# Performance work log

Measured on AMD Instinct MI355X. Metric: run time of the kernel, lower is better.

## Reference

```python
import jax, jax.numpy as jnp
import numpy as np
from jax import lax

ROI_H = 8        # _ROI_HEIGHT
MAX_BOX = 32     # generator.MAX_BOX
MAX_LEN = 64     # static cap on pooled width/height (replaces dynamic max_width)
SCALE = 8.0      # feature_map_scale
IOU_THR = 0.5    # tf.image.non_max_suppression default
SCORE_THR = 0.3
B, H, W, C = 4, 64, 64, 128


def _reconstruct_boxes(b, scale):
    # b: [B,H,W,4] per-pixel (l,t,r,b) offsets -> absolute (x1,y1,x2,y2) * scale
    Hd, Wd = b.shape[1], b.shape[2]
    xx = jnp.arange(Wd, dtype=b.dtype)[None, None, :]
    yy = jnp.arange(Hd, dtype=b.dtype)[None, :, None]
    left = xx - b[..., 0]
    top = yy - b[..., 1]
    right = xx + b[..., 2]
    bottom = yy + b[..., 3]
    return scale * jnp.stack([left, top, right, bottom], axis=-1)


def _nms_single(bbs, ss):
    # greedy NMS, bbs: [N,4] (x1,y1,x2,y2), ss: [N]; returns [MAX_BOX,4]
    x1, y1, x2, y2 = bbs[:, 0], bbs[:, 1], bbs[:, 2], bbs[:, 3]
    areas = (x2 - x1) * (y2 - y1)

    def body(i, state):
        valid, sel = state
        m = jnp.where(valid, ss, -jnp.inf)
        j = jnp.argmax(m)
        ok = m[j] > -jnp.inf
        sel = sel.at[i].set(jnp.where(ok, j.astype(jnp.int32), -1))
        bj = bbs[j]
        iw = jnp.maximum(jnp.minimum(x2, bj[2]) - jnp.maximum(x1, bj[0]), 0.0)
        ih = jnp.maximum(jnp.minimum(y2, bj[3]) - jnp.maximum(y1, bj[1]), 0.0)
        inter = iw * ih
        iou = inter / (areas + areas[j] - inter + 1e-9)
        valid = valid & (iou <= IOU_THR)   # selected box self-suppresses (iou=1)
        return valid, sel

    N = bbs.shape[0]
    valid0 = jnp.ones((N,), dtype=bool)
    sel0 = jnp.full((MAX_BOX,), -1, dtype=jnp.int32)
    _, sel = lax.fori_loop(0, MAX_BOX, body, (valid0, sel0))
    ok = sel >= 0
    idx = jnp.maximum(sel, 0)
    sb = bbs[idx]
    sc = ss[idx]
    keep = ok & (sc >= SCORE_THR)
    return jnp.where(keep[:, None], sb, jnp.zeros_like(sb))


def _bilinear(img, x, y):
    # img [H,W,C], x [Wp], y [Hp] -> [Hp,Wp,C]; matches TF clip-then-weight behavior
    Hh, Ww = img.shape[0], img.shape[1]
    x0f = jnp.floor(x)
    y0f = jnp.floor(y)
    x0 = jnp.clip(x0f.astype(jnp.int32), 0, Ww - 1)
    x1 = jnp.clip(x0f.astype(jnp.int32) + 1, 0, Ww - 1)
    y0 = jnp.clip(y0f.astype(jnp.int32), 0, Hh - 1)
    y1 = jnp.clip(y0f.astype(jnp.int32) + 1, 0, Hh - 1)
    Ia = img[y0[:, None], x0[None, :]]
    Ib = img[y0[:, None], x1[None, :]]
    Ic = img[y1[:, None], x0[None, :]]
    Id = img[y1[:, None], x1[None, :]]
    x0v, x1v = x0.astype(img.dtype), x1.astype(img.dtype)
    y0v, y1v = y0.astype(img.dtype), y1.astype(img.dtype)
    wa = (x1v - x)[None, :] * (y1v - y)[:, None]
    wb = (x1v - x)[None, :] * (y - y0v)[:, None]
    wc = (x - x0v)[None, :] * (y1v - y)[:, None]
    wd = (x - x0v)[None, :] * (y - y0v)[:, None]
    return (Ia * wa[..., None] + Ib * wb[..., None]
            + Ic * wc[..., None] + Id * wd[..., None])


def _pool_one(img, box, horizontal):
    # img [H,W,C], box [4] in feature-map coords
    w = box[2] - box[0]
    h = box[3] - box[1]
    is_dir = (w >= h) if horizontal else (w < h)
    bz = jnp.where(is_dir, box, jnp.zeros_like(box))
    w = bz[2] - bz[0]
    h = bz[3] - bz[1]
    non_zero = (w >= 0.1) | (h >= 0.1)
    bw = jnp.where(w <= 0.0, 1e-4, w)
    bh = jnp.where(h <= 0.0, 1e-4, h)
    ratio = jnp.where(non_zero, (bw / bh) if horizontal else (bh / bw), 0.0)
    n = jnp.minimum(jnp.ceil(ratio * ROI_H), float(MAX_LEN)).astype(jnp.int32)
    length_f = jnp.maximum(n.astype(img.dtype), 2.0)  # guard div-by-zero for masked boxes
    fmask = non_zero.astype(img.dtype)
    if horizontal:
        map_w = bw / (length_f - 1.0)
        map_h = bh / (ROI_H - 1.0)
        xx = jnp.arange(MAX_LEN, dtype=img.dtype) * map_w + bz[0]
        yy = jnp.arange(ROI_H, dtype=img.dtype) * map_h + bz[1]
        pooled = _bilinear(img, xx, yy)                     # [ROI_H, MAX_LEN, C]
        colmask = (jnp.arange(MAX_LEN) < n).astype(img.dtype) * fmask
        pooled = pooled * colmask[None, :, None]
    else:
        map_w = bw / (ROI_H - 1.0)
        map_h = bh / (length_f - 1.0)
        xx = jnp.arange(ROI_H, dtype=img.dtype) * map_w + bz[0]
        yy = jnp.arange(MAX_LEN, dtype=img.dtype) * map_h + bz[1]
        pooled = _bilinear(img, xx, yy)                     # [MAX_LEN, ROI_H, C]
        rowmask = (jnp.arange(MAX_LEN) < n).astype(img.dtype) * fmask
        pooled = pooled * rowmask[:, None, None]
    return pooled, n


def _roi_pool(fmap, boxes, horizontal):
    # fmap [B,H,W,C], boxes [B,M,4] -> ([B,M,...], [B,M])
    per_img = lambda img, bxs: jax.vmap(lambda b: _pool_one(img, b, horizontal))(bxs)
    return jax.vmap(per_img)(fmap, boxes)


def setup_inputs() -> dict:
    key = jax.random.key(0)
    k1, k2 = jax.random.split(key)
    fmap = jax.random.normal(k1, (B, H, W, C), dtype=jnp.float32)
    # channel 0 -> score logit, channels 1:5 -> positive l/t/r/b offsets in fmap px
    bbox_output = jax.random.uniform(k2, (B, H, W, 5), dtype=jnp.float32) * 3.0
    return {"fmap": fmap, "bbox_output": bbox_output}


def reference(fmap, bbox_output):
    scores = jax.nn.sigmoid(bbox_output[..., 0])                  # [B,H,W]
    boxes = _reconstruct_boxes(bbox_output[..., 1:5], SCALE)      # [B,H,W,4]
    Bn = scores.shape[0]
    bbs = boxes.reshape(Bn, -1, 4)
    ss = scores.reshape(Bn, -1)
    nms_boxes = jax.vmap(_nms_single)(bbs, ss)                    # [B,MAX_BOX,4]
    fb = nms_boxes / SCALE                                        # back to fmap coords
    h_roi, widths = _roi_pool(fmap, fb, True)    # [B,M,8,MAX_LEN,C], [B,M]
    v_roi, heights = _roi_pool(fmap, fb, False)  # [B,M,MAX_LEN,8,C], [B,M]
    return nms_boxes, h_roi, widths, v_roi, heights
```

## Files before the change

### kernel.cpp

```cpp
#include <hip/hip_runtime.h>
#include <hip/hip_bf16.h>
#include <math.h>

#pragma clang fp contract(off)

#define NPIX 4096
#define MAXB 32
#define NB   4
#define ROI_N 8388608
#define OTOT (ROI_N / 8)

__global__ __launch_bounds__(256) void nms_kernel(const float* __restrict__ bbox,
                                                  float* __restrict__ out_nms,
                                                  float* __restrict__ params,
                                                  float* __restrict__ out_w,
                                                  float* __restrict__ out_hh)
{
    const int b = blockIdx.x;
    const int t = threadIdx.x;

    __shared__ float s_box[NPIX][4];
    __shared__ float s_sel[MAXB][4];
    __shared__ float s_red[2][4][2];

    float rs[16], rx1[16], ry1[16], rx2[16], ry2[16], rar[16];

    const float* src = bbox + (size_t)b * NPIX * 5;

    #pragma unroll
    for (int i = 0; i < 16; ++i) {
        int p = i * 256 + t;
        int y = p >> 6, x = p & 63;
        float c0 = src[p * 5 + 0];
        float c1 = src[p * 5 + 1];
        float c2 = src[p * 5 + 2];
        float c3 = src[p * 5 + 3];
        float c4 = src[p * 5 + 4];
        float sc = 1.0f / (1.0f + expf(-c0));
        float x1 = 8.0f * ((float)x - c1);
        float y1 = 8.0f * ((float)y - c2);
        float x2 = 8.0f * ((float)x + c3);
        float y2 = 8.0f * ((float)y + c4);
        rs[i] = sc;
        rx1[i] = x1; ry1[i] = y1; rx2[i] = x2; ry2[i] = y2;
        rar[i] = (x2 - x1) * (y2 - y1);
        s_box[p][0] = x1; s_box[p][1] = y1; s_box[p][2] = x2; s_box[p][3] = y2;
    }
    __syncthreads();

    unsigned valid = 0xFFFFu;
    float wx1 = -1e30f, wy1 = -1e30f, wx2 = -1e30f, wy2 = -1e30f, warea = 0.f;

    for (int it = 0; it < MAXB; ++it) {
        float best = -INFINITY;
        int   bidx = 0x7FFFFFFF;
        #pragma unroll
        for (int i = 0; i < 16; ++i) {
            float iw = fmaxf(fminf(rx2[i], wx2) - fmaxf(rx1[i], wx1), 0.f);
            float ih = fmaxf(fminf(ry2[i], wy2) - fmaxf(ry1[i], wy1), 0.f);
            float inter = iw * ih;
            float iou = __fdiv_rn(inter, rar[i] + warea - inter + 1e-9f);
            valid &= ~(((iou > 0.5f) ? 1u : 0u) << i);
            float vv = ((valid >> i) & 1u) ? rs[i] : -INFINITY;
            bool take = vv > best;
            bidx = take ? (i * 256 + t) : bidx;
            best = take ? vv : best;
        }
        #pragma unroll
        for (int off = 32; off; off >>= 1) {
            float ov = __shfl_xor(best, off);
            int   oi = __shfl_xor(bidx, off);
            bool take = (ov > best) || (ov == best && oi < bidx);
            best = take ? ov : best;
            bidx = take ? oi : bidx;
        }
        int buf = it & 1;
        if ((t & 63) == 0) {
            s_red[buf][t >> 6][0] = best;
            s_red[buf][t >> 6][1] = __int_as_float(bidx);
        }
        __syncthreads();
        best = s_red[buf][0][0]; bidx = __float_as_int(s_red[buf][0][1]);
        #pragma unroll
        for (int wv = 1; wv < 4; ++wv) {
            float ov = s_red[buf][wv][0];
            int   oi = __float_as_int(s_red[buf][wv][1]);
            bool take = (ov > best) || (ov == best && oi < bidx);
            best = take ? ov : best;
            bidx = take ? oi : bidx;
        }

        int jj = min(bidx, NPIX - 1);
        wx1 = s_box[jj][0]; wy1 = s_box[jj][1];
        wx2 = s_box[jj][2]; wy2 = s_box[jj][3];
        warea = (wx2 - wx1) * (wy2 - wy1);

        if (t == 0) {
            bool keep = (best >= 0.3f);
            float o0 = keep ? wx1 : 0.f, o1 = keep ? wy1 : 0.f;
            float o2 = keep ? wx2 : 0.f, o3 = keep ? wy2 : 0.f;
            float* o = out_nms + ((size_t)b * MAXB + it) * 4;
            o[0] = o0; o[1] = o1; o[2] = o2; o[3] = o3;
            s_sel[it][0] = o0; s_sel[it][1] = o1;
            s_sel[it][2] = o2; s_sel[it][3] = o3;
        }
    }
    __syncthreads();

    if (t < 64) {
        int dir = t >> 5, bx = t & 31;
        float x1 = s_sel[bx][0] * 0.125f, y1 = s_sel[bx][1] * 0.125f;
        float x2 = s_sel[bx][2] * 0.125f, y2 = s_sel[bx][3] * 0.125f;
        float w = x2 - x1, h = y2 - y1;
        bool is_dir = (dir == 0) ? (w >= h) : (w < h);
        if (!is_dir) { x1 = 0.f; y1 = 0.f; x2 = 0.f; y2 = 0.f; }
        w = x2 - x1; h = y2 - y1;
        bool  non_zero = (w >= 0.1f) || (h >= 0.1f);
        float bw = (w <= 0.f) ? 1e-4f : w;
        float bh = (h <= 0.f) ? 1e-4f : h;
        float ratio = non_zero ? ((dir == 0) ? __fdiv_rn(bw, bh) : __fdiv_rn(bh, bw)) : 0.f;
        int   n = (int)fminf(ceilf(ratio * 8.0f), 64.0f);
        float length_f = fmaxf((float)n, 2.0f);
        float fmask = non_zero ? 1.f : 0.f;
        float map_w, map_h;
        if (dir == 0) { map_w = __fdiv_rn(bw, length_f - 1.0f); map_h = __fdiv_rn(bh, 7.0f); }
        else          { map_w = __fdiv_rn(bw, 7.0f);            map_h = __fdiv_rn(bh, length_f - 1.0f); }
        int gtb = b * MAXB + bx;
        float* P = params + ((size_t)dir * 128 + gtb) * 8;
        P[0] = x1; P[1] = y1; P[2] = map_w; P[3] = map_h;
        P[4] = (float)n; P[5] = fmask; P[6] = 0.f; P[7] = 0.f;
        ((dir == 0) ? out_w : out_hh)[gtb] = (float)n;
    }
}

__global__ __launch_bounds__(256) void roi_kernel(const float* __restrict__ fmap,
                                                  const float* __restrict__ params,
                                                  float* __restrict__ out_h,
                                                  float* __restrict__ out_v)
{
    int idx = blockIdx.x * 256 + threadIdx.x;
    int dir = (idx >= OTOT) ? 1 : 0;
    int e   = idx - dir * OTOT;
    int tb  = e >> 13;
    int within = e & 8191;
    int pos = within >> 4;
    int ch8 = within & 15;

    const float4* P4 = (const float4*)(params + ((size_t)dir * 128 + tb) * 8);
    float4 p0 = P4[0];
    float4 p1 = P4[1];
    float bz0x = p0.x, bz0y = p0.y, map_w = p0.z, map_h = p0.w;
    int   n     = (int)p1.x;
    float fmask = p1.y;

    int rr, cc; float mask;
    if (dir == 0) { rr = pos >> 6; cc = pos & 63; mask = (cc < n) ? fmask : 0.f; }
    else          { rr = pos >> 3; cc = pos & 7;  mask = (rr < n) ? fmask : 0.f; }

    int el = (tb << 16) | (pos << 7) | (ch8 << 3);
    float* outp = ((dir == 0) ? out_h : out_v) + el;

    if (mask == 0.f) {
        float4 z = make_float4(0.f, 0.f, 0.f, 0.f);
        *(float4*)outp = z;
        *(float4*)(outp + 4) = z;
        return;
    }

    float x = __fadd_rn(__fmul_rn((float)cc, map_w), bz0x);
    float y = __fadd_rn(__fmul_rn((float)rr, map_h), bz0y);

    float x0f = floorf(x), y0f = floorf(y);
    int ix0 = min(max((int)x0f,     0), 63);
    int ix1 = min(max((int)x0f + 1, 0), 63);
    int iy0 = min(max((int)y0f,     0), 63);
    int iy1 = min(max((int)y0f + 1, 0), 63);

    const float* img = fmap + ((size_t)(tb >> 5)) * (64 * 64 * 128) + (ch8 << 3);
    const float* pa = img + (iy0 * 64 + ix0) * 128;
    const float* pb = img + (iy0 * 64 + ix1) * 128;
    const float* pc = img + (iy1 * 64 + ix0) * 128;
    const float* pd = img + (iy1 * 64 + ix1) * 128;
    float4 Ia0 = *(const float4*)pa,       Ia1 = *(const float4*)(pa + 4);
    float4 Ib0 = *(const float4*)pb,       Ib1 = *(const float4*)(pb + 4);
    float4 Ic0 = *(const float4*)pc,       Ic1 = *(const float4*)(pc + 4);
    float4 Id0 = *(const float4*)pd,       Id1 = *(const float4*)(pd + 4);

    float x0v = (float)ix0, x1v = (float)ix1;
    float y0v = (float)iy0, y1v = (float)iy1;
    float wa = (x1v - x) * (y1v - y);
    float wb = (x1v - x) * (y - y0v);
    float wc = (x - x0v) * (y1v - y);
    float wd = (x - x0v) * (y - y0v);

    float4 o0, o1;
    o0.x = (Ia0.x * wa + Ib0.x * wb + Ic0.x * wc + Id0.x * wd) * mask;
    o0.y = (Ia0.y * wa + Ib0.y * wb + Ic0.y * wc + Id0.y * wd) * mask;
    o0.z = (Ia0.z * wa + Ib0.z * wb + Ic0.z * wc + Id0.z * wd) * mask;
    o0.w = (Ia0.w * wa + Ib0.w * wb + Ic0.w * wc + Id0.w * wd) * mask;
    o1.x = (Ia1.x * wa + Ib1.x * wb + Ic1.x * wc + Id1.x * wd) * mask;
    o1.y = (Ia1.y * wa + Ib1.y * wb + Ic1.y * wc + Id1.y * wd) * mask;
    o1.z = (Ia1.z * wa + Ib1.z * wb + Ic1.z * wc + Id1.z * wd) * mask;
    o1.w = (Ia1.w * wa + Ib1.w * wb + Ic1.w * wc + Id1.w * wd) * mask;
    *(float4*)outp = o0;
    *(float4*)(outp + 4) = o1;
}

extern "C" void kernel_launch(void* const* d_in, const int* in_sizes, int n_in,
                              void* d_out, int out_size, void* d_ws, size_t ws_size,
                              hipStream_t stream) {
    const float* fmap = (const float*)d_in[0];
    const float* bbox = (const float*)d_in[1];
    float* out = (float*)d_out;

    float* out_nms = out;
    float* out_h   = out + 512;
    float* out_w   = out_h + ROI_N;
    float* out_v   = out_w + 128;
    float* out_hh  = out_v + ROI_N;

    float* params = (float*)d_ws;

    nms_kernel<<<NB, 256, 0, stream>>>(bbox, out_nms, params, out_w, out_hh);
    roi_kernel<<<(2 * OTOT) / 256, 256, 0, stream>>>(fmap, params, out_h, out_v);
}
```

Baseline: 139.6 us.

## Use lazy per-thread NMS head tracking and nontemporal stores for ROI output

NMS no longer recomputes IoU against all 16 per-thread candidates every iteration. Each thread keeps only its current best candidate and checks it against the newly selected winner. When that candidate dies, the thread rescans its survivors and rechecks the new head against all earlier winners held in shared memory. The ROI kernel switches to ext_vector types so it can use nontemporal stores for the large output writes, which aims to cut cache pollution; this adds divergent while-loops in NMS and some risk in matching the exact suppression semantics.

```diff
diff --git a/kernel.cpp b/kernel.cpp
--- a/kernel.cpp
+++ b/kernel.cpp
@@ -9,6 +9,8 @@
 #define NB   4
 #define ROI_N 8388608
 #define OTOT (ROI_N / 8)
+
+typedef float f32x4 __attribute__((ext_vector_type(4)));
 
 __global__ __launch_bounds__(256) void nms_kernel(const float* __restrict__ bbox,
                                                   float* __restrict__ out_nms,
@@ -20,6 +22,7 @@
     const int t = threadIdx.x;
 
     __shared__ float s_box[NPIX][4];
+    __shared__ float s_win[MAXB][5];
     __shared__ float s_sel[MAXB][4];
     __shared__ float s_red[2][4][2];
 
@@ -49,23 +52,25 @@
     __syncthreads();
 
     unsigned valid = 0xFFFFu;
-    float wx1 = -1e30f, wy1 = -1e30f, wx2 = -1e30f, wy2 = -1e30f, warea = 0.f;
-
-    for (int it = 0; it < MAXB; ++it) {
-        float best = -INFINITY;
-        int   bidx = 0x7FFFFFFF;
+    float head_s; int head_p;
+    float hx1, hy1, hx2, hy2, har;
+
+    {
+        float bs = -INFINITY; int bp = 0x7FFFFFFF;
+        float b1 = 0.f, b2 = 0.f, b3 = 0.f, b4 = 0.f, ba = 0.f;
         #pragma unroll
         for (int i = 0; i < 16; ++i) {
-            float iw = fmaxf(fminf(rx2[i], wx2) - fmaxf(rx1[i], wx1), 0.f);
-            float ih = fmaxf(fminf(ry2[i], wy2) - fmaxf(ry1[i], wy1), 0.f);
-            float inter = iw * ih;
-            float iou = __fdiv_rn(inter, rar[i] + warea - inter + 1e-9f);
-            valid &= ~(((iou > 0.5f) ? 1u : 0u) << i);
-            float vv = ((valid >> i) & 1u) ? rs[i] : -INFINITY;
-            bool take = vv > best;
-            bidx = take ? (i * 256 + t) : bidx;
-            best = take ? vv : best;
-        }
+            bool take = rs[i] > bs;
+            bs = take ? rs[i] : bs; bp = take ? (i * 256 + t) : bp;
+            b1 = take ? rx1[i] : b1; b2 = take ? ry1[i] : b2;
+            b3 = take ? rx2[i] : b3; b4 = take ? ry2[i] : b4;
+            ba = take ? rar[i] : ba;
+        }
+        head_s = bs; head_p = bp; hx1 = b1; hy1 = b2; hx2 = b3; hy2 = b4; har = ba;
+    }
+
+    for (int it = 0; it < MAXB; ++it) {
+        float best = head_s; int bidx = head_p;
         #pragma unroll
         for (int off = 32; off; off >>= 1) {
             float ov = __shfl_xor(best, off);
@@ -90,10 +95,12 @@
             bidx = take ? oi : bidx;
         }
 
-        int jj = min(bidx, NPIX - 1);
-        wx1 = s_box[jj][0]; wy1 = s_box[jj][1];
-        wx2 = s_box[jj][2]; wy2 = s_box[jj][3];
-        warea = (wx2 - wx1) * (wy2 - wy1);
+        bool ok = (best > -INFINITY);
+        int  jw = bidx;
+        int  jj = min(jw, NPIX - 1);
+        float wx1 = s_box[jj][0], wy1 = s_box[jj][1];
+        float wx2 = s_box[jj][2], wy2 = s_box[jj][3];
+        float warea = (wx2 - wx1) * (wy2 - wy1);
 
         if (t == 0) {
             bool keep = (best >= 0.3f);
@@ -103,6 +110,56 @@
             o[0] = o0; o[1] = o1; o[2] = o2; o[3] = o3;
             s_sel[it][0] = o0; s_sel[it][1] = o1;
             s_sel[it][2] = o2; s_sel[it][3] = o3;
+            if (ok) {
+                s_win[it][0] = wx1; s_win[it][1] = wy1;
+                s_win[it][2] = wx2; s_win[it][3] = wy2; s_win[it][4] = warea;
+            }
+        }
+
+        if (ok && valid) {
+            bool died;
+            if (head_p == jw) {
+                died = true;
+            } else {
+                float iw = fmaxf(fminf(hx2, wx2) - fmaxf(hx1, wx1), 0.f);
+                float ih = fmaxf(fminf(hy2, wy2) - fmaxf(hy1, wy1), 0.f);
+                float inter = iw * ih;
+                died = __fdiv_rn(inter, har + warea - inter + 1e-9f) > 0.5f;
+            }
+            while (died) {
+                valid &= ~(1u << (head_p >> 8));
+                if (!valid) { head_s = -INFINITY; head_p = 0x7FFFFFFF; break; }
+                float bs = -INFINITY; int bp = 0x7FFFFFFF;
+                float b1 = 0.f, b2 = 0.f, b3 = 0.f, b4 = 0.f, ba = 0.f;
+                #pragma unroll
+                for (int i = 0; i < 16; ++i) {
+                    float vv = ((valid >> i) & 1u) ? rs[i] : -INFINITY;
+                    bool take = vv > bs;
+                    bs = take ? vv : bs; bp = take ? (i * 256 + t) : bp;
+                    b1 = take ? rx1[i] : b1; b2 = take ? ry1[i] : b2;
+                    b3 = take ? rx2[i] : b3; b4 = take ? ry2[i] : b4;
+                    ba = take ? rar[i] : ba;
+                }
+                head_s = bs; head_p = bp; hx1 = b1; hy1 = b2; hx2 = b3; hy2 = b4; har = ba;
+                {
+                    float iw = fmaxf(fminf(hx2, wx2) - fmaxf(hx1, wx1), 0.f);
+                    float ih = fmaxf(fminf(hy2, wy2) - fmaxf(hy1, wy1), 0.f);
+                    float inter = iw * ih;
+                    died = __fdiv_rn(inter, har + warea - inter + 1e-9f) > 0.5f;
+                }
+                if (!died) {
+                    for (int v = 0; v < it; ++v) {
+                        float qx1 = s_win[v][0], qy1 = s_win[v][1];
+                        float qx2 = s_win[v][2], qy2 = s_win[v][3], qa = s_win[v][4];
+                        float iw = fmaxf(fminf(hx2, qx2) - fmaxf(hx1, qx1), 0.f);
+                        float ih = fmaxf(fminf(hy2, qy2) - fmaxf(hy1, qy1), 0.f);
+                        float inter = iw * ih;
+                        if (__fdiv_rn(inter, har + qa - inter + 1e-9f) > 0.5f) {
+                            died = true; break;
+                        }
+                    }
+                }
+            }
         }
     }
     __syncthreads();
@@ -146,9 +203,9 @@
     int pos = within >> 4;
     int ch8 = within & 15;
 
-    const float4* P4 = (const float4*)(params + ((size_t)dir * 128 + tb) * 8);
-    float4 p0 = P4[0];
-    float4 p1 = P4[1];
+    const f32x4* P4 = (const f32x4*)(params + ((size_t)dir * 128 + tb) * 8);
+    f32x4 p0 = P4[0];
+    f32x4 p1 = P4[1];
     float bz0x = p0.x, bz0y = p0.y, map_w = p0.z, map_h = p0.w;
     int   n     = (int)p1.x;
     float fmask = p1.y;
@@ -161,9 +218,9 @@
     float* outp = ((dir == 0) ? out_h : out_v) + el;
 
     if (mask == 0.f) {
-        float4 z = make_float4(0.f, 0.f, 0.f, 0.f);
-        *(float4*)outp = z;
-        *(float4*)(outp + 4) = z;
+        f32x4 z = (f32x4)(0.f);
+        __builtin_nontemporal_store(z, (f32x4*)outp);
+        __builtin_nontemporal_store(z, (f32x4*)(outp + 4));
         return;
     }
 
@@ -181,10 +238,10 @@
     const float* pb = img + (iy0 * 64 + ix1) * 128;
     const float* pc = img + (iy1 * 64 + ix0) * 128;
     const float* pd = img + (iy1 * 64 + ix1) * 128;
-    float4 Ia0 = *(const float4*)pa,       Ia1 = *(const float4*)(pa + 4);
-    float4 Ib0 = *(const float4*)pb,       Ib1 = *(const float4*)(pb + 4);
-    float4 Ic0 = *(const float4*)pc,       Ic1 = *(const float4*)(pc + 4);
-    float4 Id0 = *(const float4*)pd,       Id1 = *(const float4*)(pd + 4);
+    f32x4 Ia0 = *(const f32x4*)pa,       Ia1 = *(const f32x4*)(pa + 4);
+    f32x4 Ib0 = *(const f32x4*)pb,       Ib1 = *(const f32x4*)(pb + 4);
+    f32x4 Ic0 = *(const f32x4*)pc,       Ic1 = *(const f32x4*)(pc + 4);
+    f32x4 Id0 = *(const f32x4*)pd,       Id1 = *(const f32x4*)(pd + 4);
 
     float x0v = (float)ix0, x1v = (float)ix1;
     float y0v = (float)iy0, y1v = (float)iy1;
@@ -193,7 +250,7 @@
     float wc = (x - x0v) * (y1v - y);
     float wd = (x - x0v) * (y - y0v);
 
-    float4 o0, o1;
+    f32x4 o0, o1;
     o0.x = (Ia0.x * wa + Ib0.x * wb + Ic0.x * wc + Id0.x * wd) * mask;
     o0.y = (Ia0.y * wa + Ib0.y * wb + Ic0.y * wc + Id0.y * wd) * mask;
     o0.z = (Ia0.z * wa + Ib0.z * wb + Ic0.z * wc + Id0.z * wd) * mask;
@@ -202,8 +259,8 @@
     o1.y = (Ia1.y * wa + Ib1.y * wb + Ic1.y * wc + Id1.y * wd) * mask;
     o1.z = (Ia1.z * wa + Ib1.z * wb + Ic1.z * wc + Id1.z * wd) * mask;
     o1.w = (Ia1.w * wa + Ib1.w * wb + Ic1.w * wc + Id1.w * wd) * mask;
-    *(float4*)outp = o0;
-    *(float4*)(outp + 4) = o1;
+    __builtin_nontemporal_store(o0, (f32x4*)outp);
+    __builtin_nontemporal_store(o1, (f32x4*)(outp + 4));
 }
 
 extern "C" void kernel_launch(void* const* d_in, const int* in_sizes, int n_in,
```

New measurement: 204.2 us. 1.46x slower.
